# Performance work log

Hardware: AMD Instinct MI355X
Metric: run time of the kernel (lower is better)

The kernel has to match this reference:

```python
import jax, jax.numpy as jnp
import numpy as np

N = 2048          # num_nodes
A = 100           # anchor count (hard-coded in _select_anchor_points)


def setup_inputs() -> dict:
    key = jax.random.key(0)
    k1, k2, k3 = jax.random.split(key, 3)
    motifGraph = jax.random.uniform(k1, (N, N), dtype=jnp.float32)
    node_weights = jax.random.uniform(k2, (N,), dtype=jnp.float32)
    weight_matrix = jax.random.uniform(k3, (N, A), dtype=jnp.float32)
    sigma = jnp.array(1.0, dtype=jnp.float32)
    return {"motifGraph": motifGraph, "node_weights": node_weights,
            "weight_matrix": weight_matrix, "sigma": sigma}


def _floyd_warshall(w):
    # w: [n,n] edge-weight matrix (inf = no edge, 0 on diagonal)
    n = w.shape[0]
    def step(d, k):
        # d_ij = min(d_ij, d_ik + d_kj)
        d = jnp.minimum(d, d[:, k][:, None] + d[k, :][None, :])
        return d, None
    d, _ = jax.lax.scan(step, w, jnp.arange(n))
    return d


def reference(motifGraph, node_weights, weight_matrix, sigma):
    n = motifGraph.shape[0]
    # _adjust_motif_graph: row-scale by node weights. The original detaches
    # before the scipy floyd_warshall call, so no grad flows through it.
    adj = jax.lax.stop_gradient(motifGraph * node_weights[:n, None])
    # csr_matrix semantics: zero entries are "no edge"; directed=False takes
    # the min of w_ij and w_ji; diagonal distance is 0.
    w = jnp.where(adj > 0, adj, jnp.inf)
    w = jnp.minimum(w, w.T)
    idx = jnp.arange(n)
    w = w.at[idx, idx].set(0.0)
    dist = _floyd_warshall(w)
    dist = jnp.where(jnp.isinf(dist), 100.0, dist)
    # _select_anchor_points: top-100 node weights (all indices < n here)
    anchors = jnp.argsort(-jax.lax.stop_gradient(node_weights))[:A]
    consensus_vectors = dist[:, anchors]                      # [n, A]
    distance_sums = (consensus_vectors.sum(axis=1) - 100.0).sum() / (n * A)
    weighted = weight_matrix[:n, :] * consensus_vectors       # [n, A]
    # build_consensus_graph: cdist(...)**4 == (squared euclidean dist)**2
    xx = jnp.sum(weighted * weighted, axis=1)                 # [n]
    sq = jnp.maximum(xx[:, None] + xx[None, :] - 2.0 * weighted @ weighted.T, 0.0)
    consensus_graph = jnp.exp(-(sq * sq) / (2.0 * sigma ** 2))
    return consensus_vectors, distance_sums, consensus_graph
```

## Files before the change

### kernel.cpp

```cpp
#include <hip/hip_runtime.h>
#include <stdint.h>

#define NN 2048
#define AA 100
#define NT 32

#define F_DIAG 256
#define F_ROW  512
#define F_COL  1536

template<bool AL> __device__ __forceinline__ float4 ld4(const float* __restrict__ p) {
  if (AL) return *(const float4*)p;
  return make_float4(p[0], p[1], p[2], p[3]);
}
template<bool AL> __device__ __forceinline__ void st4(float* __restrict__ p, float4 v) {
  if (AL) { *(float4*)p = v; }
  else { p[0] = v.x; p[1] = v.y; p[2] = v.z; p[3] = v.w; }
}

__device__ __forceinline__ void minplus16(const float (*A)[68], const float (*B)[68],
                                          float c[4][4], int i0, int j0) {
#pragma unroll 4
  for (int k4 = 0; k4 < 16; ++k4) {
    const int k = k4 * 4;
    float4 a0 = *(const float4*)&A[i0 + 0][k];
    float4 a1 = *(const float4*)&A[i0 + 1][k];
    float4 a2 = *(const float4*)&A[i0 + 2][k];
    float4 a3 = *(const float4*)&A[i0 + 3][k];
    float4 b0 = *(const float4*)&B[k + 0][j0];
    float4 b1 = *(const float4*)&B[k + 1][j0];
    float4 b2 = *(const float4*)&B[k + 2][j0];
    float4 b3 = *(const float4*)&B[k + 3][j0];
#define MP1(ii, jj, f)                                                           \
    c[ii][jj] = fminf(fminf(fminf(fminf(c[ii][jj], a##ii.x + b0.f),              \
                                  a##ii.y + b1.f),                               \
                            a##ii.z + b2.f),                                     \
                      a##ii.w + b3.f)
#define MP_ROW(ii) MP1(ii, 0, x); MP1(ii, 1, y); MP1(ii, 2, z); MP1(ii, 3, w)
    MP_ROW(0); MP_ROW(1); MP_ROW(2); MP_ROW(3);
#undef MP_ROW
#undef MP1
  }
}

__device__ __forceinline__ void close_seq(float (*S)[68], float c[4][4],
                                          int i0, int j0, int ty, int tx) {
  for (int kb = 0; kb < 16; ++kb) {
#pragma unroll
    for (int kq = 0; kq < 4; ++kq) {
      const int k = kb * 4 + kq;
      float4 br = *(const float4*)&S[k][j0];
      float a0 = S[i0 + 0][k];
      float a1 = S[i0 + 1][k];
      float a2 = S[i0 + 2][k];
      float a3 = S[i0 + 3][k];
      c[0][0] = fminf(c[0][0], a0 + br.x); c[0][1] = fminf(c[0][1], a0 + br.y);
      c[0][2] = fminf(c[0][2], a0 + br.z); c[0][3] = fminf(c[0][3], a0 + br.w);
      c[1][0] = fminf(c[1][0], a1 + br.x); c[1][1] = fminf(c[1][1], a1 + br.y);
      c[1][2] = fminf(c[1][2], a1 + br.z); c[1][3] = fminf(c[1][3], a1 + br.w);
      c[2][0] = fminf(c[2][0], a2 + br.x); c[2][1] = fminf(c[2][1], a2 + br.y);
      c[2][2] = fminf(c[2][2], a2 + br.z); c[2][3] = fminf(c[2][3], a2 + br.w);
      c[3][0] = fminf(c[3][0], a3 + br.x); c[3][1] = fminf(c[3][1], a3 + br.y);
      c[3][2] = fminf(c[3][2], a3 + br.z); c[3][3] = fminf(c[3][3], a3 + br.w);
      const int kn = k + 1;
      const int ii = (kq + 1) & 3;
      if (kn < 64) {
        if ((kn >> 2) == ty)
          *(float4*)&S[kn][j0] = make_float4(c[ii][0], c[ii][1], c[ii][2], c[ii][3]);
        if ((kn >> 2) == tx) {
          S[i0 + 0][kn] = c[0][ii];
          S[i0 + 1][kn] = c[1][ii];
          S[i0 + 2][kn] = c[2][ii];
          S[i0 + 3][kn] = c[3][ii];
        }
      }
      __syncthreads();
    }
  }
}

template<int LAZY>
__device__ __forceinline__ void waitflag(int* f) {
  int it = 0;
  while (__hip_atomic_load(f, __ATOMIC_RELAXED, __HIP_MEMORY_SCOPE_AGENT) == 0) {
    if (++it > 24) __builtin_amdgcn_s_sleep(LAZY);
  }
}
__device__ __forceinline__ void setflag(int* f) {
  __hip_atomic_store(f, 1, __ATOMIC_RELAXED, __HIP_MEMORY_SCOPE_AGENT);
}

__device__ __forceinline__ void stage64(const float* __restrict__ g,
                                        float (*S)[68], int t) {
#pragma unroll
  for (int l = 0; l < 4; ++l) {
    int idx = l * 256 + t;
    int row = idx >> 4, c4 = (idx & 15) * 4;
    *(float4*)&S[row][c4] = *(const float4*)&g[row * 64 + c4];
  }
}
__device__ __forceinline__ void pub64_wt(float* __restrict__ g,
                                         const float c[4][4], int i0, int j0) {
#pragma unroll
  for (int ii = 0; ii < 4; ++ii)
#pragma unroll
    for (int jj = 0; jj < 4; ++jj)
      __hip_atomic_store(&g[(i0 + ii) * 64 + j0 + jj], c[ii][jj],
                         __ATOMIC_RELAXED, __HIP_MEMORY_SCOPE_AGENT);
}

__global__ __launch_bounds__(256, 4) void fw_persist(
    const float* __restrict__ mg, const float* __restrict__ nw,
    float* __restrict__ dist, int* __restrict__ Wi,
    float* __restrict__ diagb, float* __restrict__ rowb,
    float* __restrict__ colb) {
  __shared__ __align__(16) float As[64][68];
  __shared__ __align__(16) float Bs[64][68];
  const int bx = blockIdx.x, by = blockIdx.y;
  const int t = threadIdx.x;
  const int tx = t & 15, ty = t >> 4;
  const int i0 = ty * 4, j0 = tx * 4;
  int* DIAGF = Wi + F_DIAG;
  int* ROWF  = Wi + F_ROW;
  int* COLF  = Wi + F_COL;

#pragma unroll
  for (int l = 0; l < 4; ++l) {
    int idx = l * 256 + t;
    int r = idx >> 4, c4 = (idx & 15) * 4;
    float4 g = *(const float4*)&mg[(bx * 64 + r) * NN + by * 64 + c4];
    Bs[c4 + 0][r] = g.x; Bs[c4 + 1][r] = g.y;
    Bs[c4 + 2][r] = g.z; Bs[c4 + 3][r] = g.w;
  }
  __syncthreads();
  float c[4][4];
  {
    float4 nwj = *(const float4*)&nw[bx * 64 + j0];
#pragma unroll
    for (int ii = 0; ii < 4; ++ii) {
      int rl = i0 + ii;
      int i = by * 64 + rl;
      float nwi = nw[i];
      float4 m = *(const float4*)&mg[i * NN + bx * 64 + j0];
      float4 bt = *(const float4*)&Bs[rl][j0];
      float av[4] = {m.x * nwi, m.y * nwi, m.z * nwi, m.w * nwi};
      float bv[4] = {bt.x * nwj.x, bt.y * nwj.y, bt.z * nwj.z, bt.w * nwj.w};
#pragma unroll
      for (int q = 0; q < 4; ++q) {
        float wa = av[q] > 0.0f ? av[q] : __builtin_huge_valf();
        float wb = bv[q] > 0.0f ? bv[q] : __builtin_huge_valf();
        float v = fminf(wa, wb);
        if (i == bx * 64 + j0 + q) v = 0.0f;
        c[ii][q] = v;
      }
    }
  }
  if (bx == 0 && by == 0) {
    __syncthreads();
#pragma unroll
    for (int ii = 0; ii < 4; ++ii)
      *(float4*)&As[i0 + ii][j0] = make_float4(c[ii][0], c[ii][1], c[ii][2], c[ii][3]);
    __syncthreads();
    close_seq(As, c, i0, j0, ty, tx);
    pub64_wt(diagb, c, i0, j0);
    __syncthreads();
    if (t == 0) setflag(DIAGF + 0);
  }

  for (int r = 0; r < NT; ++r) {
    if (by == r && bx == r) continue;
    if (by == r || bx == r) {
      const bool isRow = (by == r);
      __syncthreads();
      float (*Ow)[68] = isRow ? Bs : As;
#pragma unroll
      for (int ii = 0; ii < 4; ++ii)
        *(float4*)&Ow[i0 + ii][j0] =
            make_float4(c[ii][0], c[ii][1], c[ii][2], c[ii][3]);
      if (t == 0) waitflag<1>(DIAGF + r);
      __syncthreads();
      stage64(diagb + r * 4096, isRow ? As : Bs, t);
      __syncthreads();
      minplus16(As, Bs, c, i0, j0);
      float* ob = isRow ? rowb + (r * NT + bx) * 4096
                        : colb + (by * NT + r) * 4096;
      pub64_wt(ob, c, i0, j0);
      __syncthreads();
      if (t == 0) setflag(isRow ? ROWF + r * NT + bx : COLF + by * NT + r);
    } else {
      const bool closer = (bx == r + 1) && (by == r + 1) && (r + 1 < NT);
      if (closer) __builtin_amdgcn_s_setprio(1);
      if (t == 0) {
        if (closer) {
          waitflag<1>(ROWF + r * NT + bx);
          waitflag<1>(COLF + by * NT + r);
        } else {
          waitflag<8>(ROWF + r * NT + bx);
          waitflag<8>(COLF + by * NT + r);
        }
      }
      __syncthreads();
      stage64(colb + (by * NT + r) * 4096, As, t);
      stage64(rowb + (r * NT + bx) * 4096, Bs, t);
      __syncthreads();
      minplus16(As, Bs, c, i0, j0);
      if (closer) {
        __syncthreads();
#pragma unroll
        for (int ii = 0; ii < 4; ++ii)
          *(float4*)&As[i0 + ii][j0] =
              make_float4(c[ii][0], c[ii][1], c[ii][2], c[ii][3]);
        __syncthreads();
        close_seq(As, c, i0, j0, ty, tx);
        pub64_wt(diagb + (r + 1) * 4096, c, i0, j0);
        __syncthreads();
        if (t == 0) setflag(DIAGF + r + 1);
        __builtin_amdgcn_s_setprio(0);
      }
    }
  }

  float* ob = &dist[(by * 64) * NN + bx * 64];
#pragma unroll
  for (int ii = 0; ii < 4; ++ii)
    *(float4*)&ob[(i0 + ii) * NN + j0] =
        make_float4(c[ii][0], c[ii][1], c[ii][2], c[ii][3]);
}

template<bool AL>
__global__ __launch_bounds__(256) void build_w_kernel(
    const float* __restrict__ mg, const float* __restrict__ nw,
    float* __restrict__ w) {
  __shared__ float Tt[64][65];
  __shared__ __align__(16) float As[64][68];
  int bi = blockIdx.y, bj = blockIdx.x;
  int t = threadIdx.x;
  const bool diag0 = (bi == 0) && (bj == 0);
#pragma unroll
  for (int l = 0; l < 4; ++l) {
    int idx = l * 256 + t;
    int r = idx >> 4, c4 = (idx & 15) * 4;
    float4 g = *(const float4*)&mg[(bj * 64 + r) * NN + bi * 64 + c4];
    Tt[c4 + 0][r] = g.x; Tt[c4 + 1][r] = g.y;
    Tt[c4 + 2][r] = g.z; Tt[c4 + 3][r] = g.w;
  }
  __syncthreads();
#pragma unroll
  for (int l = 0; l < 4; ++l) {
    int idx = l * 256 + t;
    int r = idx >> 4, c4 = (idx & 15) * 4;
    int i = bi * 64 + r, j = bj * 64 + c4;
    float4 m = *(const float4*)&mg[i * NN + j];
    float4 nwj = *(const float4*)&nw[j];
    float nwi = nw[i];
    float av[4] = {m.x * nwi, m.y * nwi, m.z * nwi, m.w * nwi};
    float bv[4] = {Tt[r][c4 + 0] * nwj.x, Tt[r][c4 + 1] * nwj.y,
                   Tt[r][c4 + 2] * nwj.z, Tt[r][c4 + 3] * nwj.w};
    float vv[4];
#pragma unroll
    for (int q = 0; q < 4; ++q) {
      float wa = av[q] > 0.0f ? av[q] : __builtin_huge_valf();
      float wb = bv[q] > 0.0f ? bv[q] : __builtin_huge_valf();
      float v = fminf(wa, wb);
      if (i == j + q) v = 0.0f;
      vv[q] = v;
    }
    float4 v4 = make_float4(vv[0], vv[1], vv[2], vv[3]);
    if (diag0) {
      *(float4*)&As[r][c4] = v4;
    } else {
      st4<AL>(&w[i * NN + j], v4);
    }
  }
  if (diag0) {
    __syncthreads();
    int tx = t & 15, ty = t >> 4;
    int i0 = ty * 4, j0 = tx * 4;
    float c[4][4];
#pragma unroll
    for (int ii = 0; ii < 4; ++ii) {
      float4 q = *(const float4*)&As[i0 + ii][j0];
      c[ii][0] = q.x; c[ii][1] = q.y; c[ii][2] = q.z; c[ii][3] = q.w;
    }
    close_seq(As, c, i0, j0, ty, tx);
#pragma unroll
    for (int ii = 0; ii < 4; ++ii)
      st4<AL>(&w[(i0 + ii) * NN + j0],
              make_float4(c[ii][0], c[ii][1], c[ii][2], c[ii][3]));
  }
}

template<bool AL>
__global__ __launch_bounds__(256) void fw_p2(float* __restrict__ d, int r) {
  __shared__ __align__(16) float As[64][68];
  __shared__ __align__(16) float Bs[64][68];
  int tile = blockIdx.x, side = blockIdx.y;
  if (tile == r) return;
  int t = threadIdx.x;
  int dbase = (r * 64) * NN + r * 64;
  int obase = (side == 0) ? (r * 64) * NN + tile * 64
                          : (tile * 64) * NN + r * 64;
  float (*Da)[68] = (side == 0) ? As : Bs;
  float (*Ow)[68] = (side == 0) ? Bs : As;
#pragma unroll
  for (int l = 0; l < 4; ++l) {
    int idx = l * 256 + t;
    int row = idx >> 4, c4 = (idx & 15) * 4;
    *(float4*)&Da[row][c4] = ld4<AL>(&d[dbase + row * NN + c4]);
    *(float4*)&Ow[row][c4] = ld4<AL>(&d[obase + row * NN + c4]);
  }
  int tx = t & 15, ty = t >> 4;
  int i0 = ty * 4, j0 = tx * 4;
  __syncthreads();
  float c[4][4];
#pragma unroll
  for (int ii = 0; ii < 4; ++ii) {
    float4 q = *(const float4*)&Ow[i0 + ii][j0];
    c[ii][0] = q.x; c[ii][1] = q.y; c[ii][2] = q.z; c[ii][3] = q.w;
  }
  minplus16(As, Bs, c, i0, j0);
#pragma unroll
  for (int ii = 0; ii < 4; ++ii)
    st4<AL>(&d[obase + (i0 + ii) * NN + j0],
            make_float4(c[ii][0], c[ii][1], c[ii][2], c[ii][3]));
}

template<bool AL>
__global__ __launch_bounds__(256) void fw_p3(float* __restrict__ d, int r) {
  __shared__ __align__(16) float As[64][68];
  __shared__ __align__(16) float Bs[64][68];
  int bx = blockIdx.x, by = blockIdx.y;
  if (bx == r || by == r) return;
  int t = threadIdx.x;
#pragma unroll
  for (int l = 0; l < 4; ++l) {
    int idx = l * 256 + t;
    int row = idx >> 4, c4 = (idx & 15) * 4;
    *(float4*)&As[row][c4] = ld4<AL>(&d[(by * 64 + row) * NN + r * 64 + c4]);
    *(float4*)&Bs[row][c4] = ld4<AL>(&d[(r * 64 + row) * NN + bx * 64 + c4]);
  }
  int tx = t & 15, ty = t >> 4;
  int i0 = ty * 4, j0 = tx * 4;
  int obase = (by * 64) * NN + bx * 64;
  float c[4][4];
#pragma unroll
  for (int ii = 0; ii < 4; ++ii) {
    float4 q = ld4<AL>(&d[obase + (i0 + ii) * NN + j0]);
    c[ii][0] = q.x; c[ii][1] = q.y; c[ii][2] = q.z; c[ii][3] = q.w;
  }
  __syncthreads();
  minplus16(As, Bs, c, i0, j0);

  bool closer = (bx == r + 1) && (by == r + 1) && (r + 1 < NT);
  if (closer) {
    __syncthreads();
#pragma unroll
    for (int ii = 0; ii < 4; ++ii)
      *(float4*)&As[i0 + ii][j0] = make_float4(c[ii][0], c[ii][1], c[ii][2], c[ii][3]);
    __syncthreads();
    close_seq(As, c, i0, j0, ty, tx);
  }
#pragma unroll
  for (int ii = 0; ii < 4; ++ii)
    st4<AL>(&d[obase + (i0 + ii) * NN + j0],
            make_float4(c[ii][0], c[ii][1], c[ii][2], c[ii][3]));
}

__global__ __launch_bounds__(256) void anchors_kernel(
    const float* __restrict__ nw, int* __restrict__ anchors) {
  __shared__ __align__(16) float s[NN];
  int t = threadIdx.x;
#pragma unroll
  for (int l = 0; l < NN / 256; ++l) s[l * 256 + t] = nw[l * 256 + t];
  __syncthreads();
  int i = blockIdx.x * 64 + (t >> 2);
  int q = t & 3;
  float wi = s[i];
  int rank = 0;
  int jb = q * (NN / 4);
  for (int j = jb; j < jb + NN / 4; j += 4) {
    float4 v = *(const float4*)&s[j];
    rank += (int)(v.x > wi) + ((int)(v.x == wi) & (int)(j + 0 < i));
    rank += (int)(v.y > wi) + ((int)(v.y == wi) & (int)(j + 1 < i));
    rank += (int)(v.z > wi) + ((int)(v.z == wi) & (int)(j + 2 < i));
    rank += (int)(v.w > wi) + ((int)(v.w == wi) & (int)(j + 3 < i));
  }
  rank += __shfl_xor(rank, 1);
  rank += __shfl_xor(rank, 2);
  if (q == 0 && rank < AA) anchors[rank] = i;
}

__global__ __launch_bounds__(256) void cv_kernel(
    const float* __restrict__ dist, const int* __restrict__ anchors,
    float* __restrict__ cv_out, float* __restrict__ sum_acc) {
  int idx = blockIdx.x * 256 + threadIdx.x;
  int i = idx / 100, a = idx - i * 100;
  float dv = dist[i * NN + anchors[a]];
  if (isinf(dv)) dv = 100.0f;
  cv_out[idx] = dv;
  float v = dv;
#pragma unroll
  for (int off = 32; off > 0; off >>= 1) v += __shfl_down(v, off);
  __shared__ float sv[4];
  int lane = threadIdx.x & 63, w = threadIdx.x >> 6;
  if (lane == 0) sv[w] = v;
  __syncthreads();
  if (threadIdx.x == 0) atomicAdd(sum_acc, sv[0] + sv[1] + sv[2] + sv[3]);
}

__global__ __launch_bounds__(256) void graph_kernel(
    const float* __restrict__ wm, const float* __restrict__ cv,
    const float* __restrict__ sigma, float* __restrict__ graph) {
  __shared__ __align__(16) float As[64][108];
  __shared__ __align__(16) float Bs[64][108];
  __shared__ float xs[64], ys[64];
  int bx = blockIdx.x, by = blockIdx.y;
  int t = threadIdx.x;
#pragma unroll
  for (int l = 0; l < 7; ++l) {
    int idx = l * 256 + t;
    if (idx < 1600) {
      int row = idx / 25, c4 = (idx - row * 25) * 4;
      float4 wa = *(const float4*)&wm[(by * 64 + row) * AA + c4];
      float4 ca = *(const float4*)&cv[(by * 64 + row) * AA + c4];
      *(float4*)&As[row][c4] =
          make_float4(wa.x * ca.x, wa.y * ca.y, wa.z * ca.z, wa.w * ca.w);
      float4 wb = *(const float4*)&wm[(bx * 64 + row) * AA + c4];
      float4 cb = *(const float4*)&cv[(bx * 64 + row) * AA + c4];
      *(float4*)&Bs[row][c4] =
          make_float4(wb.x * cb.x, wb.y * cb.y, wb.z * cb.z, wb.w * cb.w);
    }
  }
  __syncthreads();
  if (t < 64) {
    float s = 0.0f;
    for (int k4 = 0; k4 < 25; ++k4) {
      float4 q = *(const float4*)&As[t][k4 * 4];
      s += q.x * q.x + q.y * q.y + q.z * q.z + q.w * q.w;
    }
    xs[t] = s;
  } else if (t < 128) {
    int r = t - 64;
    float s = 0.0f;
    for (int k4 = 0; k4 < 25; ++k4) {
      float4 q = *(const float4*)&Bs[r][k4 * 4];
      s += q.x * q.x + q.y * q.y + q.z * q.z + q.w * q.w;
    }
    ys[r] = s;
  }
  __syncthreads();
  int tx = t & 15, ty = t >> 4;
  float acc[4][4] = {{0.0f}};
#pragma unroll 5
  for (int k4 = 0; k4 < 25; ++k4) {
    int k = k4 * 4;
    float4 a_[4], b_[4];
#pragma unroll
    for (int ii = 0; ii < 4; ++ii) a_[ii] = *(const float4*)&As[ty + 16 * ii][k];
#pragma unroll
    for (int jj = 0; jj < 4; ++jj) b_[jj] = *(const float4*)&Bs[tx + 16 * jj][k];
#pragma unroll
    for (int ii = 0; ii < 4; ++ii)
#pragma unroll
      for (int jj = 0; jj < 4; ++jj)
        acc[ii][jj] += a_[ii].x * b_[jj].x + a_[ii].y * b_[jj].y +
                       a_[ii].z * b_[jj].z + a_[ii].w * b_[jj].w;
  }
  float s = *sigma;
  float inv2s2 = 0.5f / (s * s);
#pragma unroll
  for (int ii = 0; ii < 4; ++ii) {
    int gi = by * 64 + ty + 16 * ii;
    float xi = xs[ty + 16 * ii];
#pragma unroll
    for (int jj = 0; jj < 4; ++jj) {
      int gj = bx * 64 + tx + 16 * jj;
      float sq = fmaxf(xi + ys[tx + 16 * jj] - 2.0f * acc[ii][jj], 0.0f);
      graph[gi * NN + gj] = __expf(-(sq * sq) * inv2s2);
    }
  }
}

__global__ void finalize_kernel(const float* __restrict__ sum_acc,
                                float* __restrict__ out) {
  if (threadIdx.x == 0)
    *out = (*sum_acc - 204800.0f) / 204800.0f;
}

template<bool AL>
static void run_fw_fallback(const float* mg, const float* nw, float* dist,
                            hipStream_t stream) {
  build_w_kernel<AL><<<dim3(NT, NT), 256, 0, stream>>>(mg, nw, dist);
  for (int r = 0; r < NT; ++r) {
    fw_p2<AL><<<dim3(NT, 2), 256, 0, stream>>>(dist, r);
    fw_p3<AL><<<dim3(NT, NT), 256, 0, stream>>>(dist, r);
  }
}

static bool coop_ok() {
  static int ok = -1;
  if (ok < 0) {
    int dev = 0;
    (void)hipGetDevice(&dev);
    int coopAttr = 0;
    (void)hipDeviceGetAttribute(&coopAttr, hipDeviceAttributeCooperativeLaunch, dev);
    int cus = 0;
    (void)hipDeviceGetAttribute(&cus, hipDeviceAttributeMultiprocessorCount, dev);
    int nb = 0;
    hipError_t e = hipOccupancyMaxActiveBlocksPerMultiprocessor(&nb, fw_persist, 256, 0);
    ok = (e == hipSuccess && coopAttr && nb > 0 && (long)nb * cus >= NT * NT) ? 1 : 0;
  }
  return ok == 1;
}

extern "C" void kernel_launch(void* const* d_in, const int* in_sizes, int n_in,
                              void* d_out, int out_size, void* d_ws, size_t ws_size,
                              hipStream_t stream) {
  (void)in_sizes; (void)n_in; (void)out_size;
  const float* mg    = (const float*)d_in[0];
  const float* nw    = (const float*)d_in[1];
  const float* wm    = (const float*)d_in[2];
  const float* sigma = (const float*)d_in[3];
  float* out        = (float*)d_out;
  float* cv_out     = out;
  float* scalar_out = out + 204800;
  float* graph_out  = out + 204801;

  float* W = (float*)d_ws;
  float* sum_acc = W;
  int* anchors   = (int*)(W + 4);
  const size_t needP = (size_t)(16384 + (size_t)NN * NN + NT * 4096 +
                                2 * (size_t)NT * NT * 4096) * sizeof(float);
  const bool bigP  = ws_size >= needP;
  const bool bigF  = ws_size >= (size_t)(2048 + (size_t)NN * NN) * sizeof(float);
  float* dist = bigP ? (W + 16384) : (bigF ? (W + 2048) : graph_out);
  const bool al = ((((uintptr_t)dist) & 15) == 0);

  (void)hipMemsetAsync(W, 0, 16384, stream);

  bool launched = false;
  if (bigP && al && coop_ok()) {
    int* Wi = (int*)W;
    float* diagb = dist + (size_t)NN * NN;
    float* rowb  = diagb + NT * 4096;
    float* colb  = rowb + (size_t)NT * NT * 4096;
    void* args[] = {(void*)&mg, (void*)&nw, (void*)&dist, (void*)&Wi,
                    (void*)&diagb, (void*)&rowb, (void*)&colb};
    hipError_t ce = hipLaunchCooperativeKernel(fw_persist, dim3(NT, NT),
                                               dim3(256, 1, 1), args, 0, stream);
    launched = (ce == hipSuccess);
  }
  if (!launched) {
    if (al) run_fw_fallback<true>(mg, nw, dist, stream);
    else    run_fw_fallback<false>(mg, nw, dist, stream);
  }

  anchors_kernel<<<NN / 64, 256, 0, stream>>>(nw, anchors);
  cv_kernel<<<800, 256, 0, stream>>>(dist, anchors, cv_out, sum_acc);
  graph_kernel<<<dim3(NT, NT), 256, 0, stream>>>(wm, cv_out, sigma, graph_out);
  finalize_kernel<<<1, 64, 0, stream>>>(sum_acc, scalar_out);
}
```

Before: 1.058 ms.

## Process two pivots per barrier in diagonal closure, vectorize publishes, widen priority

```diff
diff --git a/kernel.cpp b/kernel.cpp
--- a/kernel.cpp
+++ b/kernel.cpp
@@ -8,6 +8,8 @@
 #define F_DIAG 256
 #define F_ROW  512
 #define F_COL  1536
+
+typedef float floatx4 __attribute__((ext_vector_type(4)));
 
 template<bool AL> __device__ __forceinline__ float4 ld4(const float* __restrict__ p) {
   if (AL) return *(const float4*)p;
@@ -47,31 +49,47 @@
                                           int i0, int j0, int ty, int tx) {
   for (int kb = 0; kb < 16; ++kb) {
 #pragma unroll
-    for (int kq = 0; kq < 4; ++kq) {
-      const int k = kb * 4 + kq;
-      float4 br = *(const float4*)&S[k][j0];
-      float a0 = S[i0 + 0][k];
-      float a1 = S[i0 + 1][k];
-      float a2 = S[i0 + 2][k];
-      float a3 = S[i0 + 3][k];
-      c[0][0] = fminf(c[0][0], a0 + br.x); c[0][1] = fminf(c[0][1], a0 + br.y);
-      c[0][2] = fminf(c[0][2], a0 + br.z); c[0][3] = fminf(c[0][3], a0 + br.w);
-      c[1][0] = fminf(c[1][0], a1 + br.x); c[1][1] = fminf(c[1][1], a1 + br.y);
-      c[1][2] = fminf(c[1][2], a1 + br.z); c[1][3] = fminf(c[1][3], a1 + br.w);
-      c[2][0] = fminf(c[2][0], a2 + br.x); c[2][1] = fminf(c[2][1], a2 + br.y);
-      c[2][2] = fminf(c[2][2], a2 + br.z); c[2][3] = fminf(c[2][3], a2 + br.w);
-      c[3][0] = fminf(c[3][0], a3 + br.x); c[3][1] = fminf(c[3][1], a3 + br.y);
-      c[3][2] = fminf(c[3][2], a3 + br.z); c[3][3] = fminf(c[3][3], a3 + br.w);
-      const int kn = k + 1;
-      const int ii = (kq + 1) & 3;
+    for (int h = 0; h < 2; ++h) {
+      const int k = kb * 4 + h * 2;
+      float4 br  = *(const float4*)&S[k][j0];
+      float4 br2 = *(const float4*)&S[k + 1][j0];
+      float dkk1 = S[k][k + 1];
+      float dk1k = S[k + 1][k];
+      float a0 = S[i0 + 0][k],     a1 = S[i0 + 1][k],
+            a2 = S[i0 + 2][k],     a3 = S[i0 + 3][k];
+      float e0 = S[i0 + 0][k + 1], e1 = S[i0 + 1][k + 1],
+            e2 = S[i0 + 2][k + 1], e3 = S[i0 + 3][k + 1];
+      float4 brp;
+      brp.x = fminf(br2.x, dk1k + br.x);
+      brp.y = fminf(br2.y, dk1k + br.y);
+      brp.z = fminf(br2.z, dk1k + br.z);
+      brp.w = fminf(br2.w, dk1k + br.w);
+      e0 = fminf(e0, a0 + dkk1);
+      e1 = fminf(e1, a1 + dkk1);
+      e2 = fminf(e2, a2 + dkk1);
+      e3 = fminf(e3, a3 + dkk1);
+#define CS2(ii, aa, ee)                                                     \
+      c[ii][0] = fminf(fminf(c[ii][0], aa + br.x), ee + brp.x);             \
+      c[ii][1] = fminf(fminf(c[ii][1], aa + br.y), ee + brp.y);             \
+      c[ii][2] = fminf(fminf(c[ii][2], aa + br.z), ee + brp.z);             \
+      c[ii][3] = fminf(fminf(c[ii][3], aa + br.w), ee + brp.w)
+      CS2(0, a0, e0); CS2(1, a1, e1); CS2(2, a2, e2); CS2(3, a3, e3);
+#undef CS2
+      const int kn = k + 2;
       if (kn < 64) {
-        if ((kn >> 2) == ty)
-          *(float4*)&S[kn][j0] = make_float4(c[ii][0], c[ii][1], c[ii][2], c[ii][3]);
-        if ((kn >> 2) == tx) {
-          S[i0 + 0][kn] = c[0][ii];
-          S[i0 + 1][kn] = c[1][ii];
-          S[i0 + 2][kn] = c[2][ii];
-          S[i0 + 3][kn] = c[3][ii];
+        const int ow = kn >> 2;
+        const int ri = (h == 0) ? 2 : 0;
+        if (ow == ty) {
+          *(float4*)&S[kn][j0] =
+              make_float4(c[ri][0], c[ri][1], c[ri][2], c[ri][3]);
+          *(float4*)&S[kn + 1][j0] =
+              make_float4(c[ri + 1][0], c[ri + 1][1], c[ri + 1][2], c[ri + 1][3]);
+        }
+        if (ow == tx) {
+          S[i0 + 0][kn] = c[0][ri]; S[i0 + 0][kn + 1] = c[0][ri + 1];
+          S[i0 + 1][kn] = c[1][ri]; S[i0 + 1][kn + 1] = c[1][ri + 1];
+          S[i0 + 2][kn] = c[2][ri]; S[i0 + 2][kn + 1] = c[2][ri + 1];
+          S[i0 + 3][kn] = c[3][ri]; S[i0 + 3][kn + 1] = c[3][ri + 1];
         }
       }
       __syncthreads();
@@ -102,11 +120,13 @@
 __device__ __forceinline__ void pub64_wt(float* __restrict__ g,
                                          const float c[4][4], int i0, int j0) {
 #pragma unroll
-  for (int ii = 0; ii < 4; ++ii)
-#pragma unroll
-    for (int jj = 0; jj < 4; ++jj)
-      __hip_atomic_store(&g[(i0 + ii) * 64 + j0 + jj], c[ii][jj],
-                         __ATOMIC_RELAXED, __HIP_MEMORY_SCOPE_AGENT);
+  for (int ii = 0; ii < 4; ++ii) {
+    floatx4 v = {c[ii][0], c[ii][1], c[ii][2], c[ii][3]};
+    float* p = &g[(i0 + ii) * 64 + j0];
+    asm volatile("global_store_dwordx4 %0, %1, off sc0 sc1"
+                 :: "v"(p), "v"(v) : "memory");
+  }
+  asm volatile("s_waitcnt vmcnt(0)" ::: "memory");
 }
 
 __global__ __launch_bounds__(256, 4) void fw_persist(
@@ -168,6 +188,9 @@
   }
 
   for (int r = 0; r < NT; ++r) {
+    const bool crit = (by == r) || (bx == r) || (by == r + 1) || (bx == r + 1);
+    if (crit) __builtin_amdgcn_s_setprio(1);
+    else      __builtin_amdgcn_s_setprio(0);
     if (by == r && bx == r) continue;
     if (by == r || bx == r) {
       const bool isRow = (by == r);
@@ -189,9 +212,8 @@
       if (t == 0) setflag(isRow ? ROWF + r * NT + bx : COLF + by * NT + r);
     } else {
       const bool closer = (bx == r + 1) && (by == r + 1) && (r + 1 < NT);
-      if (closer) __builtin_amdgcn_s_setprio(1);
       if (t == 0) {
-        if (closer) {
+        if (crit) {
           waitflag<1>(ROWF + r * NT + bx);
           waitflag<1>(COLF + by * NT + r);
         } else {
@@ -215,10 +237,10 @@
         pub64_wt(diagb + (r + 1) * 4096, c, i0, j0);
         __syncthreads();
         if (t == 0) setflag(DIAGF + r + 1);
-        __builtin_amdgcn_s_setprio(0);
       }
     }
   }
+  __builtin_amdgcn_s_setprio(0);
 
   float* ob = &dist[(by * 64) * NN + bx * 64];
 #pragma unroll
```

After: 921.7 us. 1.15x faster.
